# Kernel optimization log

Hardware: AMD Instinct MI355X
Metric: run time of the kernel (lower is better)

The kernel has to match this reference:

```python
import jax, jax.numpy as jnp
import numpy as np

B, T, SIG, MET, H, F, OUT = 256, 128, 64, 32, 256, 16, 1
TWO_PI = float(2.0 * np.pi)


def setup_inputs() -> dict:
    key = jax.random.key(0)
    ks = jax.random.split(key, 24)
    rn = lambda k, s, sc=0.05: jax.random.normal(k, s, jnp.float32) * sc
    return {
        "signal": rn(ks[0], (B, T, SIG), 1.0),
        "metmast": rn(ks[1], (B, T, MET), 1.0),
        "W_i_signal": rn(ks[2], (SIG, H)),
        "W_ste_signal": rn(ks[3], (SIG, H)),
        "W_fre_signal": rn(ks[4], (SIG, F)),
        "W_c_signal": rn(ks[5], (SIG, H)),
        "W_o_signal": rn(ks[6], (SIG, H)),
        "W_i_metmast": rn(ks[7], (MET, H)),
        "W_ste_metmast": rn(ks[8], (MET, H)),
        "W_fre_metmast": rn(ks[9], (MET, F)),
        "W_c_metmast": rn(ks[10], (MET, H)),
        "W_o_metmast": rn(ks[11], (MET, H)),
        "U_i": rn(ks[12], (H, H)),
        "b_i": jnp.zeros((H,), jnp.float32),
        "U_ste": rn(ks[13], (H, H)),
        "b_ste": jnp.ones((H,), jnp.float32),
        "U_fre": rn(ks[14], (H, F)),
        "b_fre": jnp.ones((F,), jnp.float32),
        "U_c": rn(ks[15], (H, H)),
        "b_c": jnp.zeros((H,), jnp.float32),
        "U_o": rn(ks[16], (H, H)),
        "b_o": jnp.zeros((H,), jnp.float32),
        "U_a": rn(ks[17], (F, 1)),
        "b_a": jnp.zeros((H,), jnp.float32),
        "W_p": rn(ks[18], (H, OUT)),
        "b_p": jnp.zeros((OUT,), jnp.float32),
        "fc_w": rn(ks[19], (OUT, OUT), 0.5),
        "fc_b": jnp.zeros((OUT,), jnp.float32),
    }


def _hsig(x):
    # torch.nn.Hardsigmoid: clip(x/6 + 0.5, 0, 1)
    return jnp.clip(x / 6.0 + 0.5, 0.0, 1.0)


def reference(signal, metmast, W_i_signal, W_ste_signal, W_fre_signal, W_c_signal,
              W_o_signal, W_i_metmast, W_ste_metmast, W_fre_metmast, W_c_metmast,
              W_o_metmast, U_i, b_i, U_ste, b_ste, U_fre, b_fre, U_c, b_c, U_o, b_o,
              U_a, b_a, W_p, b_p, fc_w, fc_b):
    Bn, Tn, _ = signal.shape
    Hn, Fn = U_i.shape[0], U_a.shape[0]
    freq = jnp.arange(Fn, dtype=jnp.float32) / Fn  # [F]
    sig_t = jnp.swapaxes(signal, 0, 1)   # [T, B, SIG]
    met_t = jnp.swapaxes(metmast, 0, 1)  # [T, B, MET]

    def step(carry, x):
        h, S_re, S_im, t = carry
        xs, xm = x
        x_i = xs @ W_i_signal + xm @ W_i_metmast + b_i
        x_ste = xs @ W_ste_signal + xm @ W_ste_metmast + b_ste
        x_fre = xs @ W_fre_signal + xm @ W_fre_metmast + b_fre
        x_c = xs @ W_c_signal + xm @ W_c_metmast + b_c
        x_o = xs @ W_o_signal + xm @ W_o_metmast + b_o
        i = _hsig(x_i + h @ U_i)                # [B,H]
        ste = _hsig(x_ste + h @ U_ste)          # [B,H]
        fre = _hsig(x_fre + h @ U_fre)          # [B,F]
        f = ste[:, :, None] * fre[:, None, :]   # [B,H,F] forget gate
        c = i * jnp.tanh(x_c + h @ U_c)         # [B,H]
        t = t + 1.0
        omega = TWO_PI * t * freq               # [F]
        re, im = jnp.cos(omega), jnp.sin(omega)
        c3 = c[:, :, None]
        S_re = f * S_re + c3 * re
        S_im = f * S_im + c3 * im
        A = S_re * S_re + S_im * S_im           # [B,H,F] amplitude
        A_a = jnp.einsum('bhf,f->bh', A, U_a[:, 0])
        a = jnp.tanh(A_a + b_a)
        o = _hsig(x_o + h @ U_o)
        h = o * a
        return (h, S_re, S_im, t), None

    S0 = jnp.zeros((Bn, Hn, Fn), jnp.float32)
    carry0 = (jnp.zeros((Bn, Hn), jnp.float32), S0, S0, jnp.float32(0.0))
    (h, _, _, _), _ = jax.lax.scan(step, carry0, (sig_t, met_t))
    p = h @ W_p + b_p                # [B, OUT] (last timestep only is used)
    out = p @ fc_w.T + fc_b          # fc_out
    return out.squeeze()
```

## Files before the change

kernel.cpp:

```cpp
#include <hip/hip_runtime.h>
#include <hip/hip_fp16.h>
#include <cstdint>
#include <cstddef>

#define B_    256
#define T_    128
#define SIG_  64
#define MET_  32
#define H_    256
#define F_    16
#define NCOL  1040

#define NLDS  3

__device__ __forceinline__ float hsig(float x) {
    return fminf(fmaxf(x * (1.0f/6.0f) + 0.5f, 0.0f), 1.0f);
}

__device__ __forceinline__ unsigned short f2h(float f) {
    __half h = __float2half(f);
    return *(unsigned short*)&h;
}

__device__ __forceinline__ float ntload_f(const float* p) {
    return __builtin_nontemporal_load(p);
}
__device__ __forceinline__ float4 ntload_f4(const float* p) {
    float4 v;
    v.x = __builtin_nontemporal_load(p + 0);
    v.y = __builtin_nontemporal_load(p + 1);
    v.z = __builtin_nontemporal_load(p + 2);
    v.w = __builtin_nontemporal_load(p + 3);
    return v;
}

__device__ __forceinline__ void lbar() {
    asm volatile("s_waitcnt lgkmcnt(0)\n\ts_barrier" ::: "memory");
}

typedef _Float16 half2v __attribute__((ext_vector_type(2)));

__device__ __forceinline__ float dot2(unsigned int u, unsigned int h, float acc) {
#if __has_builtin(__builtin_amdgcn_fdot2)
    return __builtin_amdgcn_fdot2(__builtin_bit_cast(half2v, u),
                                  __builtin_bit_cast(half2v, h), acc, false);
#else
    __half2 uu = *(__half2*)&u, hh = *(__half2*)&h;
    float2 uf = __half22float2(uu), hf = __half22float2(hh);
    return fmaf(uf.x, hf.x, fmaf(uf.y, hf.y, acc));
#endif
}

__device__ __forceinline__ float dot2x4(uint4 u, uint4 h, float acc) {
    acc = dot2(u.x, h.x, acc);
    acc = dot2(u.y, h.y, acc);
    acc = dot2(u.z, h.z, acc);
    acc = dot2(u.w, h.w, acc);
    return acc;
}

__global__ __launch_bounds__(256) void pack_kernel(
    const float* __restrict__ Wis, const float* __restrict__ Wstes, const float* __restrict__ Wfres,
    const float* __restrict__ Wcs, const float* __restrict__ Wos,
    const float* __restrict__ Wim, const float* __restrict__ Wstem, const float* __restrict__ Wfrem,
    const float* __restrict__ Wcm, const float* __restrict__ Wom,
    const float* __restrict__ Ui, const float* __restrict__ Uste, const float* __restrict__ Ufre,
    const float* __restrict__ Uc, const float* __restrict__ Uo,
    const float* __restrict__ bi, const float* __restrict__ bste, const float* __restrict__ bfre,
    const float* __restrict__ bc, const float* __restrict__ bo,
    float* __restrict__ Wcat, float* __restrict__ bcat,
    unsigned short* __restrict__ U8, unsigned short* __restrict__ UF)
{
    int gtid = blockIdx.x * blockDim.x + threadIdx.x;
    int stride = gridDim.x * blockDim.x;
    const float* Wsig[5] = {Wis, Wstes, Wcs, Wos, Wfres};
    const float* Wmet[5] = {Wim, Wstem, Wcm, Wom, Wfrem};
    const float* Us[4]   = {Ui, Uste, Uc, Uo};
    const float* bs[5]   = {bi, bste, bc, bo, bfre};

    for (int i = gtid; i < 96*NCOL; i += stride) {
        int k = i / NCOL, n = i - k*NCOL;
        int sec, idx, secN;
        if (n < 1024) { sec = n >> 8; idx = n & 255; secN = H_; }
        else          { sec = 4; idx = n - 1024; secN = F_; }
        float v = (k < 64) ? Wsig[sec][k*secN + idx] : Wmet[sec][(k-64)*secN + idx];
        Wcat[k*NCOL + n] = v;
    }
    for (int n = gtid; n < NCOL; n += stride) {
        int sec, idx;
        if (n < 1024) { sec = n >> 8; idx = n & 255; }
        else          { sec = 4; idx = n - 1024; }
        bcat[n] = bs[sec][idx];
    }
    for (int i = gtid; i < 1024*H_; i += stride) {
        int col = i >> 8, k = i & 255;
        int sec = col >> 8, idx = col & 255;
        U8[(((k >> 3) * 1024) + col) * 8 + (k & 7)] = f2h(Us[sec][k*H_ + idx]);
    }
    for (int i = gtid; i < 16*H_; i += stride) {
        int col = i >> 8, k = i & 255;
        UF[col*H_ + k] = f2h(Ufre[k*F_ + col]);
    }
}

__global__ __launch_bounds__(256) void proj_kernel(
    const float* __restrict__ sig, const float* __restrict__ met,
    const float* __restrict__ Wcat, const float* __restrict__ bcat,
    float* __restrict__ X)
{
    __shared__ float A_s[32][128];
    __shared__ float W_s[32][128];
    int tid = threadIdx.x;
    int c0b = blockIdx.x * 128;
    int m0  = blockIdx.y * 128;
    int t0  = blockIdx.z * 16;
    int r0  = (tid >> 4) * 8;
    int c0t = (tid & 15) * 8;

    float acc[8][8];
    #pragma unroll
    for (int i = 0; i < 8; ++i)
        #pragma unroll
        for (int j = 0; j < 8; ++j) acc[i][j] = 0.0f;

    for (int k0 = 0; k0 < 96; k0 += 32) {
        for (int idx = tid; idx < 32*128; idx += 256) {
            int ml = idx & 127, kk = idx >> 7;
            int m = m0 + ml;
            int b = m >> 4, tl = m & 15;
            int g = b * T_ + t0 + tl;
            int k = k0 + kk;
            float v = (k < 64) ? sig[g*SIG_ + k] : met[g*MET_ + (k - 64)];
            A_s[kk][ml] = v;
        }
        for (int idx = tid; idx < 32*128; idx += 256) {
            int c = idx & 127, kk = idx >> 7;
            int n = c0b + c;
            W_s[kk][c] = (n < NCOL) ? Wcat[(k0+kk)*NCOL + n] : 0.0f;
        }
        __syncthreads();
        #pragma unroll
        for (int kk = 0; kk < 32; ++kk) {
            float4 a0 = *(const float4*)&A_s[kk][r0];
            float4 a1 = *(const float4*)&A_s[kk][r0+4];
            float4 w0 = *(const float4*)&W_s[kk][c0t];
            float4 w1 = *(const float4*)&W_s[kk][c0t+4];
            float av[8] = {a0.x,a0.y,a0.z,a0.w,a1.x,a1.y,a1.z,a1.w};
            float wv[8] = {w0.x,w0.y,w0.z,w0.w,w1.x,w1.y,w1.z,w1.w};
            #pragma unroll
            for (int i = 0; i < 8; ++i)
                #pragma unroll
                for (int j = 0; j < 8; ++j)
                    acc[i][j] = fmaf(av[i], wv[j], acc[i][j]);
        }
        __syncthreads();
    }
    #pragma unroll
    for (int i = 0; i < 8; ++i) {
        int m = m0 + r0 + i;
        int bb = m >> 4, tl = m & 15;
        size_t row = (size_t)bb * T_ + t0 + tl;
        #pragma unroll
        for (int j = 0; j < 8; ++j) {
            int n = c0b + c0t + j;
            if (n < NCOL) X[row*NCOL + n] = acc[i][j] + bcat[n];
        }
    }
}

__global__ __launch_bounds__(1024) void recur_kernel(
    const float* __restrict__ X, const uint4* __restrict__ U8,
    const uint4* __restrict__ UF,
    const float* __restrict__ U_a, const float* __restrict__ b_a,
    const float* __restrict__ W_p, const float* __restrict__ b_p,
    const float* __restrict__ fc_w, const float* __restrict__ fc_b,
    float* __restrict__ out)
{
    __shared__ uint4 ldsU[NLDS * 1024];
    __shared__ float pre_s[1024];
    __shared__ uint4 h_p4[H_/8];
    __shared__ float qp[64];
    __shared__ float cs_s[16], sn_s[16];

    int tid  = threadIdx.x;
    int b    = blockIdx.x;
    int lane = tid & 63;
    int wid  = tid >> 6;
    bool isfre = ((lane & 15) == 15);
    int fq = lane >> 4;

    int j  = tid >> 2;
    int f0 = (tid & 3) * 4;

    #pragma unroll
    for (int d = 0; d < NLDS; ++d)
        ldsU[d * 1024 + tid] = U8[d * 1024 + tid];

    if (tid < H_/8) { uint4 z; z.x=z.y=z.z=z.w=0u; h_p4[tid] = z; }
    if (tid < 16) {
        float ang = (float)tid * 0.39269908169872414f;
        cs_s[tid] = cosf(ang);
        sn_s[tid] = sinf(ang);
    }
    float Sre[4], Sim[4];
    #pragma unroll
    for (int r = 0; r < 4; ++r) { Sre[r] = 0.0f; Sim[r] = 0.0f; }

    float ba_j = b_a[j];
    float4 ua4 = ((const float4*)U_a)[tid & 3];
    const uint4* Uf = UF + (wid * 32 + fq * 8);
    const float* Xb = X + (size_t)b * T_ * NCOL;
    __half* h_h = (__half*)h_p4;

    float hnew = 0.0f;
    __syncthreads();

    for (int t = 0; t < T_; ++t) {
        const float* xrow = Xb + (size_t)t * NCOL;

        float acc = ntload_f(&xrow[tid]);
        #pragma unroll 8
        for (int kk = NLDS; kk < 32; ++kk) {
            uint4 u = U8[kk * 1024 + tid];
            acc = dot2x4(u, h_p4[kk], acc);
        }
        #pragma unroll
        for (int d = 0; d < NLDS; ++d) {
            uint4 u = ldsU[d * 1024 + tid];
            acc = dot2x4(u, h_p4[d], acc);
        }
        float fa = 0.0f;
        if (isfre) {
            #pragma unroll
            for (int q = 0; q < 8; ++q)
                fa = dot2x4(Uf[q], h_p4[fq * 8 + q], fa);
        }
        pre_s[tid] = acc;
        if (isfre) qp[wid*4 + fq] = fa;
        lbar();

        float xi   = pre_s[j];
        float xste = pre_s[256 + j];
        float xc   = pre_s[512 + j];
        float xo   = pre_s[768 + j];
        float gi   = hsig(xi);
        float gste = hsig(xste);
        float go   = hsig(xo);
        float cc   = gi * tanhf(xc);

        float4 xfre = ntload_f4(&xrow[1024 + f0]);
        float4 q0 = *(const float4*)&qp[(f0+0)*4];
        float4 q1 = *(const float4*)&qp[(f0+1)*4];
        float4 q2 = *(const float4*)&qp[(f0+2)*4];
        float4 q3 = *(const float4*)&qp[(f0+3)*4];
        float fre[4];
        fre[0] = hsig(xfre.x + q0.x + q0.y + q0.z + q0.w);
        fre[1] = hsig(xfre.y + q1.x + q1.y + q1.z + q1.w);
        fre[2] = hsig(xfre.z + q2.x + q2.y + q2.z + q2.w);
        fre[3] = hsig(xfre.w + q3.x + q3.y + q3.z + q3.w);

        int tt1 = (t + 1) & 15;
        float Aa = 0.0f;
        #pragma unroll
        for (int r = 0; r < 4; ++r) {
            int idx = (tt1 * (f0 + r)) & 15;
            float dec = gste * fre[r];
            float sre = fmaf(dec, Sre[r], cc * cs_s[idx]);
            float sim = fmaf(dec, Sim[r], cc * sn_s[idx]);
            Sre[r] = sre; Sim[r] = sim;
            Aa = fmaf(fmaf(sre, sre, sim*sim), ((const float*)&ua4)[r], Aa);
        }
        Aa += __shfl_xor(Aa, 1);
        Aa += __shfl_xor(Aa, 2);
        if ((tid & 3) == 0) {
            float a = tanhf(Aa + ba_j);
            hnew = go * a;
            h_h[j] = __float2half(hnew);
        }
        lbar();
    }

    if ((tid & 3) == 0) pre_s[j] = hnew * W_p[j];
    __syncthreads();
    for (int s = 128; s > 0; s >>= 1) {
        if (tid < s) pre_s[tid] += pre_s[tid + s];
        __syncthreads();
    }
    if (tid == 0) out[b] = (pre_s[0] + b_p[0]) * fc_w[0] + fc_b[0];
}

extern "C" void kernel_launch(void* const* d_in, const int* in_sizes, int n_in,
                              void* d_out, int out_size, void* d_ws, size_t ws_size,
                              hipStream_t stream) {
    const float* signal = (const float*)d_in[0];
    const float* metmast = (const float*)d_in[1];
    const float* W_i_s   = (const float*)d_in[2];
    const float* W_ste_s = (const float*)d_in[3];
    const float* W_fre_s = (const float*)d_in[4];
    const float* W_c_s   = (const float*)d_in[5];
    const float* W_o_s   = (const float*)d_in[6];
    const float* W_i_m   = (const float*)d_in[7];
    const float* W_ste_m = (const float*)d_in[8];
    const float* W_fre_m = (const float*)d_in[9];
    const float* W_c_m   = (const float*)d_in[10];
    const float* W_o_m   = (const float*)d_in[11];
    const float* U_i   = (const float*)d_in[12];
    const float* b_i   = (const float*)d_in[13];
    const float* U_ste = (const float*)d_in[14];
    const float* b_ste = (const float*)d_in[15];
    const float* U_fre = (const float*)d_in[16];
    const float* b_fre = (const float*)d_in[17];
    const float* U_c   = (const float*)d_in[18];
    const float* b_c   = (const float*)d_in[19];
    const float* U_o   = (const float*)d_in[20];
    const float* b_o   = (const float*)d_in[21];
    const float* U_a   = (const float*)d_in[22];
    const float* b_a   = (const float*)d_in[23];
    const float* W_p   = (const float*)d_in[24];
    const float* b_p   = (const float*)d_in[25];
    const float* fc_w  = (const float*)d_in[26];
    const float* fc_b  = (const float*)d_in[27];
    float* out = (float*)d_out;

    char* ws = (char*)d_ws;
    float*          Wcat = (float*)(ws + 0);
    float*          bcat = (float*)(ws + 399360);
    unsigned short* U8   = (unsigned short*)(ws + 403520);
    unsigned short* UF   = (unsigned short*)(ws + 927808);
    float*          X    = (float*)(ws + 936000);

    pack_kernel<<<256, 256, 0, stream>>>(
        W_i_s, W_ste_s, W_fre_s, W_c_s, W_o_s,
        W_i_m, W_ste_m, W_fre_m, W_c_m, W_o_m,
        U_i, U_ste, U_fre, U_c, U_o,
        b_i, b_ste, b_fre, b_c, b_o,
        Wcat, bcat, U8, UF);

    proj_kernel<<<dim3(9, 32, 8), 256, 0, stream>>>(signal, metmast, Wcat, bcat, X);

    recur_kernel<<<B_, 1024, 0, stream>>>(X, (const uint4*)U8, (const uint4*)UF,
                                          U_a, b_a, W_p, b_p, fc_w, fc_b, out);
}
```

Measured before the change: 1.074 ms.

## Stream recurrent weights as scaled FP8 E4M3 instead of FP16

The recurrent U weights streamed from global memory each timestep (k-blocks beyond the LDS-resident ones) are quantized to FP8 E4M3 with a 64x scale in the pack kernel. In the recurrence they are unpacked to half2 and accumulated with fdot2, then rescaled and added to the main accumulator. This halves the per-step global/L2 traffic for the weight stream, at the cost of extra conversion instructions and a precision loss that may break numerical tolerance over 128 recurrent steps.

```diff
diff --git a/kernel.cpp b/kernel.cpp
--- a/kernel.cpp
+++ b/kernel.cpp
@@ -12,6 +12,16 @@
 #define NCOL  1040
 
 #define NLDS  3
+#define NSTRM (32 - NLDS)
+
+#if __has_builtin(__builtin_amdgcn_cvt_pk_f32_fp8) && __has_builtin(__builtin_amdgcn_cvt_pk_fp8_f32) && __has_builtin(__builtin_amdgcn_cvt_pkrtz)
+#define HAVE_FP8 1
+#else
+#define HAVE_FP8 0
+#endif
+
+typedef float  f2v  __attribute__((ext_vector_type(2)));
+typedef _Float16 half2v __attribute__((ext_vector_type(2)));
 
 __device__ __forceinline__ float hsig(float x) {
     return fminf(fmaxf(x * (1.0f/6.0f) + 0.5f, 0.0f), 1.0f);
@@ -37,8 +47,6 @@
 __device__ __forceinline__ void lbar() {
     asm volatile("s_waitcnt lgkmcnt(0)\n\ts_barrier" ::: "memory");
 }
-
-typedef _Float16 half2v __attribute__((ext_vector_type(2)));
 
 __device__ __forceinline__ float dot2(unsigned int u, unsigned int h, float acc) {
 #if __has_builtin(__builtin_amdgcn_fdot2)
@@ -57,6 +65,34 @@
     acc = dot2(u.z, h.z, acc);
     acc = dot2(u.w, h.w, acc);
     return acc;
+}
+
+template <bool HI>
+__device__ __forceinline__ unsigned int fp8pair2h2(unsigned int w) {
+#if HAVE_FP8
+    f2v f = __builtin_amdgcn_cvt_pk_f32_fp8((int)w, HI);
+    auto h = __builtin_amdgcn_cvt_pkrtz(f.x, f.y);
+    return __builtin_bit_cast(unsigned int, h);
+#else
+    unsigned int bsel = HI ? (w >> 16) : (w & 0xffffu);
+    unsigned int sp = ((bsel & 0xffu) << 8) | ((bsel & 0xff00u) << 16);
+    return (sp & 0x80008000u) | (((sp & 0x7f007f00u) >> 1) + 0x20002000u);
+#endif
+}
+
+__device__ __forceinline__ unsigned int f2e4m3(float x) {
+#if HAVE_FP8
+    return (unsigned int)(__builtin_amdgcn_cvt_pk_fp8_f32(x, x, 0, false) & 0xff);
+#else
+    unsigned int bb = __float_as_uint(x);
+    unsigned int s = (bb >> 24) & 0x80u;
+    unsigned int m = bb & 0x7fffffffu;
+    if (m < 0x3c800000u) return s | 0x08u;
+    unsigned int r = m + 0x7ffffu + ((m >> 20) & 1u);
+    int ee = (int)(r >> 23) - 120;
+    if (ee > 15) return s | 0x7eu;
+    return s | ((unsigned int)ee << 3) | ((r >> 20) & 7u);
+#endif
 }
 
 __global__ __launch_bounds__(256) void pack_kernel(
@@ -69,7 +105,8 @@
     const float* __restrict__ bi, const float* __restrict__ bste, const float* __restrict__ bfre,
     const float* __restrict__ bc, const float* __restrict__ bo,
     float* __restrict__ Wcat, float* __restrict__ bcat,
-    unsigned short* __restrict__ U8, unsigned short* __restrict__ UF)
+    unsigned short* __restrict__ U8, unsigned short* __restrict__ UQ,
+    unsigned short* __restrict__ UF)
 {
     int gtid = blockIdx.x * blockDim.x + threadIdx.x;
     int stride = gridDim.x * blockDim.x;
@@ -92,10 +129,20 @@
         else          { sec = 4; idx = n - 1024; }
         bcat[n] = bs[sec][idx];
     }
-    for (int i = gtid; i < 1024*H_; i += stride) {
-        int col = i >> 8, k = i & 255;
+    for (int i = gtid; i < 1024*24; i += stride) {
+        int col = i & 1023, k = i >> 10;
         int sec = col >> 8, idx = col & 255;
         U8[(((k >> 3) * 1024) + col) * 8 + (k & 7)] = f2h(Us[sec][k*H_ + idx]);
+    }
+    for (int i = gtid; i < 1024*116; i += stride) {
+        int col = i & 1023, pi = i >> 10;
+        int k0 = 24 + 2*pi;
+        int kk = k0 >> 3, p = (k0 & 7) >> 1;
+        int sec = col >> 8, idx = col & 255;
+        float v0 = Us[sec][k0*H_ + idx] * 64.0f;
+        float v1 = Us[sec][(k0+1)*H_ + idx] * 64.0f;
+        UQ[(((kk - NLDS) * 1024) + col) * 4 + p] =
+            (unsigned short)(f2e4m3(v0) | (f2e4m3(v1) << 8));
     }
     for (int i = gtid; i < 16*H_; i += stride) {
         int col = i >> 8, k = i & 255;
@@ -170,7 +217,7 @@
 
 __global__ __launch_bounds__(1024) void recur_kernel(
     const float* __restrict__ X, const uint4* __restrict__ U8,
-    const uint4* __restrict__ UF,
+    const uint2* __restrict__ UQ, const uint4* __restrict__ UF,
     const float* __restrict__ U_a, const float* __restrict__ b_a,
     const float* __restrict__ W_p, const float* __restrict__ b_p,
     const float* __restrict__ fc_w, const float* __restrict__ fc_b,
@@ -218,17 +265,24 @@
     for (int t = 0; t < T_; ++t) {
         const float* xrow = Xb + (size_t)t * NCOL;
 
-        float acc = ntload_f(&xrow[tid]);
+        float acc  = ntload_f(&xrow[tid]);
+        float accq = 0.0f;
         #pragma unroll 8
         for (int kk = NLDS; kk < 32; ++kk) {
-            uint4 u = U8[kk * 1024 + tid];
-            acc = dot2x4(u, h_p4[kk], acc);
+            uint2 u = UQ[(kk - NLDS) * 1024 + tid];
+            uint4 hp = h_p4[kk];
+            accq = dot2(fp8pair2h2<false>(u.x), hp.x, accq);
+            accq = dot2(fp8pair2h2<true >(u.x), hp.y, accq);
+            accq = dot2(fp8pair2h2<false>(u.y), hp.z, accq);
+            accq = dot2(fp8pair2h2<true >(u.y), hp.w, accq);
         }
         #pragma unroll
         for (int d = 0; d < NLDS; ++d) {
             uint4 u = ldsU[d * 1024 + tid];
             acc = dot2x4(u, h_p4[d], acc);
         }
+        acc = fmaf(accq, 0.015625f, acc);
+
         float fa = 0.0f;
         if (isfre) {
             #pragma unroll
@@ -326,18 +380,20 @@
     float*          Wcat = (float*)(ws + 0);
     float*          bcat = (float*)(ws + 399360);
     unsigned short* U8   = (unsigned short*)(ws + 403520);
-    unsigned short* UF   = (unsigned short*)(ws + 927808);
-    float*          X    = (float*)(ws + 936000);
+    unsigned short* UQ   = (unsigned short*)(ws + 452672);
+    unsigned short* UF   = (unsigned short*)(ws + 690240);
+    float*          X    = (float*)(ws + 698432);
 
     pack_kernel<<<256, 256, 0, stream>>>(
         W_i_s, W_ste_s, W_fre_s, W_c_s, W_o_s,
         W_i_m, W_ste_m, W_fre_m, W_c_m, W_o_m,
         U_i, U_ste, U_fre, U_c, U_o,
         b_i, b_ste, b_fre, b_c, b_o,
-        Wcat, bcat, U8, UF);
+        Wcat, bcat, U8, UQ, UF);
 
     proj_kernel<<<dim3(9, 32, 8), 256, 0, stream>>>(signal, metmast, Wcat, bcat, X);
 
-    recur_kernel<<<B_, 1024, 0, stream>>>(X, (const uint4*)U8, (const uint4*)UF,
+    recur_kernel<<<B_, 1024, 0, stream>>>(X, (const uint4*)U8, (const uint2*)UQ,
+                                          (const uint4*)UF,
                                           U_a, b_a, W_p, b_p, fc_w, fc_b, out);
 }
```

Result: no change. 1.083 ms (+0.8%).
